# Optimization experiments

Hardware: AMD Instinct MI355X
Metric: run time of the kernel (lower is better)

Reference implementation:

```python
import jax, jax.numpy as jnp
import numpy as np

N, E, MB, H, FA, FB, HEADS, A_SIZE = 60000, 120000, 6, 128, 133, 147, 8, 20


def setup_inputs() -> dict:
    key = jax.random.key(0)
    ks = jax.random.split(key, 32)
    nrm = lambda k, s, sc: (jax.random.normal(k, s, jnp.float32) * sc)
    HD = HEADS * H
    inp = {
        "f_atoms": jax.random.normal(ks[0], (N, FA), jnp.float32),
        "f_bonds": jax.random.normal(ks[1], (E, FB), jnp.float32),
        "wi_atom": nrm(ks[2], (H, FA), 1 / np.sqrt(FA)),
        "wi_bond": nrm(ks[3], (H, FB), 1 / np.sqrt(FB)),
        "wh0": nrm(ks[4], (H, H), 1 / np.sqrt(H)),
        "wh1": nrm(ks[5], (H, H), 1 / np.sqrt(H)),
        "wh2": nrm(ks[6], (H, H), 1 / np.sqrt(H)),
        "q_w": nrm(ks[7], (HD, H), 1 / np.sqrt(H)),
        "q_b": nrm(ks[8], (HD,), 0.02),
        "k_w": nrm(ks[9], (HD, H), 1 / np.sqrt(H)),
        "k_b": nrm(ks[10], (HD,), 0.02),
        "v_w": nrm(ks[11], (HD, H), 1 / np.sqrt(H)),
        "v_b": nrm(ks[12], (HD,), 0.02),
        "e_w": nrm(ks[13], (HD, H), 1 / np.sqrt(H)),
        "skip_w": nrm(ks[14], (H, H), 1 / np.sqrt(H)),
        "skip_b": nrm(ks[15], (H,), 0.02),
        "lstm_wih": nrm(ks[16], (4 * H, 2 * H), 1 / np.sqrt(H)),
        "lstm_whh": nrm(ks[17], (4 * H, H), 1 / np.sqrt(H)),
        "lstm_bih": nrm(ks[18], (4 * H,), 1 / np.sqrt(H)),
        "lstm_bhh": nrm(ks[19], (4 * H,), 1 / np.sqrt(H)),
        "wo_w": nrm(ks[20], (H, 2 * H), 1 / np.sqrt(2 * H)),
        "wo_b": nrm(ks[21], (H,), 0.02),
        "a2b": jax.random.randint(ks[22], (N, MB), 0, E),
        "b2a": jax.random.randint(ks[23], (E,), 0, N),
        "b2revb": jax.random.randint(ks[24], (E,), 0, E),
        "bonds": jax.random.randint(ks[25], (2, E), 0, N),
        "a_size": A_SIZE,
    }
    return inp


def reference(f_atoms, f_bonds, wi_atom, wi_bond, wh0, wh1, wh2, q_w, q_b, k_w, k_b,
              v_w, v_b, e_w, skip_w, skip_b, lstm_wih, lstm_whh, lstm_bih, lstm_bhh,
              wo_w, wo_b, a2b, b2a, b2revb, bonds, a_size):
    relu = jax.nn.relu
    n = f_atoms.shape[0]
    h = wi_atom.shape[0]
    heads = q_w.shape[0] // h
    # input projections (bias=False) + activation
    input_atom = relu(f_atoms @ wi_atom.T)
    message_atom = input_atom
    input_bond = relu(f_bonds @ wi_bond.T)
    message_bond = input_bond
    # depth-1 = 3 message passing iterations (dropout p=0 -> identity)
    for wh in (wh0, wh1, wh2):
        nei = message_bond[a2b]                    # [N, max_nb, H] gather
        agg = nei.sum(axis=1) * nei.max(axis=1)    # fused sum*max aggregation
        message_atom = message_atom + agg
        mb = message_atom[b2a] - message_bond[b2revb]
        message_bond = relu(input_bond + mb @ wh.T)
    # TransformerConv(H, H, heads=8, concat=False, edge_dim=H)
    src, dst = bonds[0], bonds[1]
    e_num = src.shape[0]
    q = (message_atom @ q_w.T + q_b).reshape(n, heads, h)
    k = (message_atom @ k_w.T + k_b).reshape(n, heads, h)
    v = (message_atom @ v_w.T + v_b).reshape(n, heads, h)
    eattr = (message_bond @ e_w.T).reshape(e_num, heads, h)
    k_j = k[src] + eattr
    v_j = v[src] + eattr
    logits = (q[dst] * k_j).sum(-1) / jnp.sqrt(jnp.float32(h))  # [E, heads]
    m = jax.ops.segment_max(logits, dst, num_segments=n)
    m = jnp.where(jnp.isfinite(m), m, 0.0)
    ex = jnp.exp(logits - m[dst])
    denom = jax.ops.segment_sum(ex, dst, num_segments=n) + 1e-16
    alpha = ex / denom[dst]
    out = jax.ops.segment_sum(v_j * alpha[..., None], dst, num_segments=n)
    atom_hiddens = out.mean(axis=1) + (message_atom @ skip_w.T + skip_b)
    # Set2Set(T=1, num_layers=1) per molecule, vectorized over equal-size mols
    m_mols = n // a_size
    x = atom_hiddens.reshape(m_mols, a_size, h)
    hh = jnp.zeros((m_mols, h), jnp.float32)
    cc = jnp.zeros((m_mols, h), jnp.float32)
    q_star = jnp.zeros((m_mols, 2 * h), jnp.float32)
    gates = q_star @ lstm_wih.T + lstm_bih + hh @ lstm_whh.T + lstm_bhh
    gi, gf, gg, go = jnp.split(gates, 4, axis=-1)  # torch LSTM gate order i,f,g,o
    cc = jax.nn.sigmoid(gf) * cc + jax.nn.sigmoid(gi) * jnp.tanh(gg)
    qv = jax.nn.sigmoid(go) * jnp.tanh(cc)          # [M, H]
    e_att = (x * qv[:, None, :]).sum(-1)            # [M, A]
    a = jnp.exp(e_att - e_att.max(axis=1, keepdims=True))
    a = a / (a.sum(axis=1, keepdims=True) + 1e-16)
    r = jnp.einsum('ma,mah->mh', a, x)
    q_star = jnp.concatenate([qv, r], axis=-1)      # [M, 2H]
    return q_star @ wo_w.T + wo_b                   # [M, H]
```

## Files before the change

### kernel.cpp

```cpp
#include <hip/hip_runtime.h>
#include <hip/hip_bf16.h>

__global__ void zero_u32(unsigned int* __restrict__ p, long long n)
{
    long long i = (long long)blockIdx.x * 256 + threadIdx.x;
    if (i < n) p[i] = 0u;
}

__global__ void sentinel_f32(float* __restrict__ p, long long n, float v)
{
    long long i = (long long)blockIdx.x * 256 + threadIdx.x;
    if (i < n) p[i] = v;
}

__device__ __forceinline__ float4 load_f4_guard(const float* base, int gm, int M, int K, int kb)
{
    float4 v = make_float4(0.f, 0.f, 0.f, 0.f);
    if (gm < M) {
        const float* p = base + (size_t)gm * K + kb;
        if (kb + 4 <= K) v = *(const float4*)p;
        else {
            if (kb     < K) v.x = p[0];
            if (kb + 1 < K) v.y = p[1];
            if (kb + 2 < K) v.z = p[2];
            if (kb + 3 < K) v.w = p[3];
        }
    }
    return v;
}

struct GSeg {
    const float* A; const float* W; const float* bias; float* C;
    int M; int K; int bend;
};
struct GParams { GSeg s[4]; };

template<bool RELU>
__global__ __launch_bounds__(256) void gemm_multi(GParams P, int nseg)
{
    __shared__ float As[16][68];
    __shared__ float Ws[16][132];
    const int b = blockIdx.x;
    int si = 0, bbeg = 0;
    while (si + 1 < nseg && b >= P.s[si].bend) { bbeg = P.s[si].bend; ++si; }
    const GSeg S = P.s[si];
    const int tid = threadIdx.x;
    const int tx = tid & 15, ty = tid >> 4;
    const int row0 = (b - bbeg) * 64;
    const int r  = tid >> 2;
    const int k4 = (tid & 3) * 4;

    float acc[4][8] = {};
    for (int k0 = 0; k0 < S.K; k0 += 16) {
        {
            float4 av = load_f4_guard(S.A, row0 + r, S.M, S.K, k0 + k4);
            As[k4 + 0][r] = av.x; As[k4 + 1][r] = av.y;
            As[k4 + 2][r] = av.z; As[k4 + 3][r] = av.w;
        }
#pragma unroll
        for (int c = 0; c < 2; ++c) {
            int rr = r + c * 64;
            float4 wv = load_f4_guard(S.W, rr, 128, S.K, k0 + k4);
            Ws[k4 + 0][rr] = wv.x; Ws[k4 + 1][rr] = wv.y;
            Ws[k4 + 2][rr] = wv.z; Ws[k4 + 3][rr] = wv.w;
        }
        __syncthreads();
#pragma unroll
        for (int kk = 0; kk < 16; ++kk) {
            float4 a0 = *(const float4*)&As[kk][ty * 4];
            float4 w0 = *(const float4*)&Ws[kk][tx * 4];
            float4 w1 = *(const float4*)&Ws[kk][64 + tx * 4];
            float a[4] = {a0.x, a0.y, a0.z, a0.w};
            float w[8] = {w0.x, w0.y, w0.z, w0.w, w1.x, w1.y, w1.z, w1.w};
#pragma unroll
            for (int i = 0; i < 4; ++i)
#pragma unroll
                for (int j = 0; j < 8; ++j)
                    acc[i][j] += a[i] * w[j];
        }
        __syncthreads();
    }
    float bs[8];
    if (S.bias) {
#pragma unroll
        for (int j = 0; j < 4; ++j) {
            bs[j]     = S.bias[tx * 4 + j];
            bs[j + 4] = S.bias[64 + tx * 4 + j];
        }
    } else {
#pragma unroll
        for (int j = 0; j < 8; ++j) bs[j] = 0.f;
    }
#pragma unroll
    for (int i = 0; i < 4; ++i) {
        int gm = row0 + ty * 4 + i;
        if (gm >= S.M) continue;
#pragma unroll
        for (int jh = 0; jh < 2; ++jh) {
            float4 v;
            v.x = acc[i][jh * 4 + 0] + bs[jh * 4 + 0];
            v.y = acc[i][jh * 4 + 1] + bs[jh * 4 + 1];
            v.z = acc[i][jh * 4 + 2] + bs[jh * 4 + 2];
            v.w = acc[i][jh * 4 + 3] + bs[jh * 4 + 3];
            if (RELU) {
                v.x = fmaxf(v.x, 0.f); v.y = fmaxf(v.y, 0.f);
                v.z = fmaxf(v.z, 0.f); v.w = fmaxf(v.w, 0.f);
            }
            *(float4*)&S.C[(size_t)gm * 128 + jh * 64 + tx * 4] = v;
        }
    }
}

__global__ __launch_bounds__(256) void gemm_mp(
    const float* __restrict__ ma, const float* __restrict__ bond,
    const int* __restrict__ b2a, const int* __restrict__ b2revb,
    const float* __restrict__ inb, const float* __restrict__ wh,
    float* __restrict__ C)
{
    __shared__ float As[16][68];
    __shared__ float Ws[16][132];
    __shared__ int ia[64], ir[64];
    const int tid = threadIdx.x;
    const int tx = tid & 15, ty = tid >> 4;
    const int row0 = blockIdx.x * 64;
    const int r  = tid >> 2;
    const int k4 = (tid & 3) * 4;
    if (tid < 64)       ia[tid]      = b2a[row0 + tid];
    else if (tid < 128) ir[tid - 64] = b2revb[row0 + tid - 64];
    __syncthreads();
    float acc[4][8] = {};
    for (int k0 = 0; k0 < 128; k0 += 16) {
        {
            float4 x = *(const float4*)(ma   + (size_t)ia[r] * 128 + k0 + k4);
            float4 y = *(const float4*)(bond + (size_t)ir[r] * 128 + k0 + k4);
            As[k4 + 0][r] = x.x - y.x; As[k4 + 1][r] = x.y - y.y;
            As[k4 + 2][r] = x.z - y.z; As[k4 + 3][r] = x.w - y.w;
        }
#pragma unroll
        for (int c = 0; c < 2; ++c) {
            int rr = r + c * 64;
            float4 wv = *(const float4*)(wh + (size_t)rr * 128 + k0 + k4);
            Ws[k4 + 0][rr] = wv.x; Ws[k4 + 1][rr] = wv.y;
            Ws[k4 + 2][rr] = wv.z; Ws[k4 + 3][rr] = wv.w;
        }
        __syncthreads();
#pragma unroll
        for (int kk = 0; kk < 16; ++kk) {
            float4 a0 = *(const float4*)&As[kk][ty * 4];
            float4 w0 = *(const float4*)&Ws[kk][tx * 4];
            float4 w1 = *(const float4*)&Ws[kk][64 + tx * 4];
            float a[4] = {a0.x, a0.y, a0.z, a0.w};
            float w[8] = {w0.x, w0.y, w0.z, w0.w, w1.x, w1.y, w1.z, w1.w};
#pragma unroll
            for (int i = 0; i < 4; ++i)
#pragma unroll
                for (int j = 0; j < 8; ++j)
                    acc[i][j] += a[i] * w[j];
        }
        __syncthreads();
    }
#pragma unroll
    for (int i = 0; i < 4; ++i) {
        int gm = row0 + ty * 4 + i;
#pragma unroll
        for (int jh = 0; jh < 2; ++jh) {
            int cc = jh * 64 + tx * 4;
            float4 o = *(const float4*)&inb[(size_t)gm * 128 + cc];
            float4 v;
            v.x = fmaxf(acc[i][jh * 4 + 0] + o.x, 0.f);
            v.y = fmaxf(acc[i][jh * 4 + 1] + o.y, 0.f);
            v.z = fmaxf(acc[i][jh * 4 + 2] + o.z, 0.f);
            v.w = fmaxf(acc[i][jh * 4 + 3] + o.w, 0.f);
            *(float4*)&C[(size_t)gm * 128 + cc] = v;
        }
    }
}

__global__ __launch_bounds__(256) void agg_kernel(
    const float* __restrict__ bond, const int* __restrict__ a2b,
    float* __restrict__ ma, int N)
{
    int n = blockIdx.x * 8 + (threadIdx.x >> 5);
    if (n >= N) return;
    int d4 = (threadIdx.x & 31) * 4;
    const int* ix = a2b + (size_t)n * 6;
    float4 s = make_float4(0.f, 0.f, 0.f, 0.f);
    float4 mx = make_float4(-3.0e38f, -3.0e38f, -3.0e38f, -3.0e38f);
#pragma unroll
    for (int j = 0; j < 6; ++j) {
        float4 v = *(const float4*)(bond + (size_t)ix[j] * 128 + d4);
        s.x += v.x; s.y += v.y; s.z += v.z; s.w += v.w;
        mx.x = fmaxf(mx.x, v.x); mx.y = fmaxf(mx.y, v.y);
        mx.z = fmaxf(mx.z, v.z); mx.w = fmaxf(mx.w, v.w);
    }
    float* mp = ma + (size_t)n * 128 + d4;
    float4 o = *(const float4*)mp;
    o.x += s.x * mx.x; o.y += s.y * mx.y; o.z += s.z * mx.z; o.w += s.w * mx.w;
    *(float4*)mp = o;
}

__global__ void count_kernel(const int* __restrict__ dst, int* __restrict__ counts, int E)
{
    int e = blockIdx.x * 256 + threadIdx.x;
    if (e < E) atomicAdd(&counts[dst[e]], 1);
}

__global__ __launch_bounds__(1024) void scan_kernel(
    const int* __restrict__ counts, int* __restrict__ offsets, int N)
{
    __shared__ int sums[1024];
    int t = threadIdx.x;
    int chunk = (N + 1023) >> 10;
    int b = t * chunk;
    int e = b + chunk; if (e > N) e = N;
    int s = 0;
    for (int i = b; i < e; ++i) s += counts[i];
    sums[t] = s;
    __syncthreads();
    for (int off = 1; off < 1024; off <<= 1) {
        int v = (t >= off) ? sums[t - off] : 0;
        __syncthreads();
        sums[t] += v;
        __syncthreads();
    }
    int run = sums[t] - s;
    for (int i = b; i < e; ++i) { offsets[i] = run; run += counts[i]; }
    if (t == 1023) offsets[N] = sums[1023];
}

__global__ void fill_kernel(const int* __restrict__ dst, const int* __restrict__ offsets,
                            int* __restrict__ cursor, int* __restrict__ elist, int E)
{
    int e = blockIdx.x * 256 + threadIdx.x;
    if (e < E) {
        int d = dst[e];
        int pos = offsets[d] + atomicAdd(&cursor[d], 1);
        elist[pos] = e;
    }
}

__global__ __launch_bounds__(256) void attn_pass1(
    const float* __restrict__ qh, const float* __restrict__ kh,
    const float* __restrict__ eh, const int* __restrict__ srcA,
    const int* __restrict__ offs, const int* __restrict__ elist,
    float* __restrict__ alpha, int N)
{
    int n = blockIdx.x * 4 + (threadIdx.x >> 6);
    if (n >= N) return;
    int l = threadIdx.x & 63;
    const float rs = 0.08838834764831845f;
    float2 q2 = ((const float2*)(qh + (size_t)n * 128))[l];
    int b = offs[n], en = offs[n + 1];
    float m = -3.0e38f, denom = 0.f;
    int ie = b;
    for (; ie + 2 <= en; ie += 2) {
        int e0 = elist[ie], e1 = elist[ie + 1];
        int s0 = srcA[e0], s1 = srcA[e1];
        float2 k0v = ((const float2*)(kh + (size_t)s0 * 128))[l];
        float2 e0v = ((const float2*)(eh + (size_t)e0 * 128))[l];
        float2 k1v = ((const float2*)(kh + (size_t)s1 * 128))[l];
        float2 e1v = ((const float2*)(eh + (size_t)e1 * 128))[l];
        float p0 = q2.x * (k0v.x + e0v.x) + q2.y * (k0v.y + e0v.y);
        float p1 = q2.x * (k1v.x + e1v.x) + q2.y * (k1v.y + e1v.y);
        p0 += __shfl_xor(p0, 1);  p1 += __shfl_xor(p1, 1);
        p0 += __shfl_xor(p0, 2);  p1 += __shfl_xor(p1, 2);
        p0 += __shfl_xor(p0, 4);  p1 += __shfl_xor(p1, 4);
        p0 += __shfl_xor(p0, 8);  p1 += __shfl_xor(p1, 8);
        p0 += __shfl_xor(p0, 16); p1 += __shfl_xor(p1, 16);
        p0 += __shfl_xor(p0, 32); p1 += __shfl_xor(p1, 32);
        float l0 = p0 * rs, l1 = p1 * rs;
        if (l == 0) { alpha[ie] = l0; alpha[ie + 1] = l1; }
        float mn = fmaxf(m, fmaxf(l0, l1));
        float sc = __expf(m - mn);
        denom = denom * sc + __expf(l0 - mn) + __expf(l1 - mn);
        m = mn;
    }
    if (ie < en) {
        int e0 = elist[ie];
        int s0 = srcA[e0];
        float2 k0v = ((const float2*)(kh + (size_t)s0 * 128))[l];
        float2 e0v = ((const float2*)(eh + (size_t)e0 * 128))[l];
        float p0 = q2.x * (k0v.x + e0v.x) + q2.y * (k0v.y + e0v.y);
        p0 += __shfl_xor(p0, 1);  p0 += __shfl_xor(p0, 2);
        p0 += __shfl_xor(p0, 4);  p0 += __shfl_xor(p0, 8);
        p0 += __shfl_xor(p0, 16); p0 += __shfl_xor(p0, 32);
        float l0 = p0 * rs;
        if (l == 0) alpha[ie] = l0;
        float mn = fmaxf(m, l0);
        denom = denom * __expf(m - mn) + __expf(l0 - mn);
        m = mn;
    }
    if (l == 0 && b < en) {
        float invd = 1.f / (denom + 1e-16f);
        for (int i = b; i < en; ++i)
            alpha[i] = __expf(alpha[i] - m) * invd;
    }
}

__global__ __launch_bounds__(256) void attn_pass2(
    const float* __restrict__ vh, const float* __restrict__ eh,
    const int* __restrict__ srcA, const int* __restrict__ offs,
    const int* __restrict__ elist, const float* __restrict__ alpha,
    float* __restrict__ outsum, int N)
{
    int n = blockIdx.x * 4 + (threadIdx.x >> 6);
    if (n >= N) return;
    int l = threadIdx.x & 63;
    int b = offs[n], en = offs[n + 1];
    float a0 = 0.f, a1 = 0.f;
    int ie = b;
    for (; ie + 2 <= en; ie += 2) {
        int e0 = elist[ie], e1 = elist[ie + 1];
        int s0 = srcA[e0], s1 = srcA[e1];
        float al0 = alpha[ie], al1 = alpha[ie + 1];
        float2 v0 = ((const float2*)(vh + (size_t)s0 * 128))[l];
        float2 e0v = ((const float2*)(eh + (size_t)e0 * 128))[l];
        float2 v1 = ((const float2*)(vh + (size_t)s1 * 128))[l];
        float2 e1v = ((const float2*)(eh + (size_t)e1 * 128))[l];
        a0 += al0 * (v0.x + e0v.x) + al1 * (v1.x + e1v.x);
        a1 += al0 * (v0.y + e0v.y) + al1 * (v1.y + e1v.y);
    }
    if (ie < en) {
        int e0 = elist[ie];
        int s0 = srcA[e0];
        float al0 = alpha[ie];
        float2 v0 = ((const float2*)(vh + (size_t)s0 * 128))[l];
        float2 e0v = ((const float2*)(eh + (size_t)e0 * 128))[l];
        a0 += al0 * (v0.x + e0v.x);
        a1 += al0 * (v0.y + e0v.y);
    }
    float* op = outsum + (size_t)n * 128 + 2 * l;
    op[0] += 0.125f * a0;
    op[1] += 0.125f * a1;
}

__global__ void qv_kernel(const float* __restrict__ bih, const float* __restrict__ bhh,
                          float* __restrict__ qv)
{
    int t = threadIdx.x;
    float gi = bih[t] + bhh[t];
    float gg = bih[256 + t] + bhh[256 + t];
    float go = bih[384 + t] + bhh[384 + t];
    float sig_i = 1.f / (1.f + __expf(-gi));
    float c = sig_i * tanhf(gg);
    float sig_o = 1.f / (1.f + __expf(-go));
    qv[t] = sig_o * tanhf(c);
}

__global__ __launch_bounds__(256) void s2s_kernel(
    const float* __restrict__ ah, const float* __restrict__ qv,
    const float* __restrict__ wo_w, const float* __restrict__ wo_b,
    float* __restrict__ out, int M)
{
    __shared__ float rsh[4][128];
    __shared__ float qsh[128];
    int wv = threadIdx.x >> 6, l = threadIdx.x & 63;
    if (threadIdx.x < 128) qsh[threadIdx.x] = qv[threadIdx.x];
    __syncthreads();
    int m = blockIdx.x * 4 + wv;
    bool active = (m < M);
    if (active) {
        const float* x = ah + (size_t)m * 20 * 128;
        float q0 = qsh[2 * l], q1 = qsh[2 * l + 1];
        float e[20]; float mx = -3.0e38f;
#pragma unroll
        for (int a = 0; a < 20; ++a) {
            float part = x[a * 128 + 2 * l] * q0 + x[a * 128 + 2 * l + 1] * q1;
            part += __shfl_xor(part, 1);  part += __shfl_xor(part, 2);
            part += __shfl_xor(part, 4);  part += __shfl_xor(part, 8);
            part += __shfl_xor(part, 16); part += __shfl_xor(part, 32);
            e[a] = part; mx = fmaxf(mx, part);
        }
        float sum = 0.f;
#pragma unroll
        for (int a = 0; a < 20; ++a) { e[a] = __expf(e[a] - mx); sum += e[a]; }
        float invs = 1.f / (sum + 1e-16f);
        float r0 = 0.f, r1 = 0.f;
#pragma unroll
        for (int a = 0; a < 20; ++a) {
            float w = e[a] * invs;
            r0 += w * x[a * 128 + 2 * l];
            r1 += w * x[a * 128 + 2 * l + 1];
        }
        rsh[wv][2 * l] = r0; rsh[wv][2 * l + 1] = r1;
    }
    __syncthreads();
    if (active) {
#pragma unroll
        for (int dd = 0; dd < 2; ++dd) {
            int d = 2 * l + dd;
            float acc = wo_b[d];
            const float* wr = wo_w + (size_t)d * 256;
            for (int j = 0; j < 128; ++j)
                acc += wr[j] * qsh[j] + wr[128 + j] * rsh[wv][j];
            out[(size_t)m * 128 + d] = acc;
        }
    }
}

extern "C" void kernel_launch(void* const* d_in, const int* in_sizes, int n_in,
                              void* d_out, int out_size, void* d_ws, size_t ws_size,
                              hipStream_t stream)
{
    const int N = 60000, E = 120000, FA = 133, FB = 147;
    const float* f_atoms  = (const float*)d_in[0];
    const float* f_bonds  = (const float*)d_in[1];
    const float* wi_atom  = (const float*)d_in[2];
    const float* wi_bond  = (const float*)d_in[3];
    const float* wh[3]    = { (const float*)d_in[4], (const float*)d_in[5], (const float*)d_in[6] };
    const float* q_w      = (const float*)d_in[7];
    const float* q_b      = (const float*)d_in[8];
    const float* k_w      = (const float*)d_in[9];
    const float* k_b      = (const float*)d_in[10];
    const float* v_w      = (const float*)d_in[11];
    const float* v_b      = (const float*)d_in[12];
    const float* e_w      = (const float*)d_in[13];
    const float* skip_w   = (const float*)d_in[14];
    const float* skip_b   = (const float*)d_in[15];
    const float* lstm_bih = (const float*)d_in[18];
    const float* lstm_bhh = (const float*)d_in[19];
    const float* wo_w     = (const float*)d_in[20];
    const float* wo_b     = (const float*)d_in[21];
    const int* a2b    = (const int*)d_in[22];
    const int* b2a    = (const int*)d_in[23];
    const int* b2revb = (const int*)d_in[24];
    const int* bonds  = (const int*)d_in[25];
    const int* srcA = bonds;
    const int* dstA = bonds + E;

    const size_t NB = (size_t)N * 128;
    const size_t EB = (size_t)E * 128;
    char* ws = (char*)d_ws;
    size_t off = 0;
    auto alloc = [&](size_t bytes) -> char* {
        char* p = ws + off; off += (bytes + 255) & ~255ULL; return p;
    };
    float* msg_atom = (float*)alloc(NB * 4);
    float* B1       = (float*)alloc(EB * 4);
    float* B2       = (float*)alloc(EB * 4);
    float* B3       = (float*)alloc(EB * 4);
    float* outsum   = (float*)alloc(NB * 4);
    float* alpha    = (float*)alloc((size_t)E * 4);
    int* counts  = (int*)alloc((size_t)N * 2 * 4);
    int* cursor  = counts + N;
    int* offsets = (int*)alloc((size_t)(N + 1) * 4);
    int* elist   = (int*)alloc((size_t)E * 4);
    float* qvb   = (float*)alloc(128 * 4);

    if (off > ws_size) {
        long long n = out_size;
        sentinel_f32<<<(int)((n + 255) / 256), 256, 0, stream>>>((float*)d_out, n, 1.0e9f);
        return;
    }

    float* q_h = B1;
    float* k_h = B1 + NB;
    float* v_h = B1;
    float* e_h = B3;

    const int gN64 = (N + 63) / 64;
    const int gE64 = E / 64;

    zero_u32<<<(2 * N + 255) / 256, 256, 0, stream>>>((unsigned int*)counts, 2 * N);

    {
        GParams P{};
        P.s[0] = { f_atoms, wi_atom, nullptr, msg_atom, N, FA, gN64 };
        P.s[1] = { f_bonds, wi_bond, nullptr, B1,       E, FB, gN64 + gE64 };
        gemm_multi<true><<<gN64 + gE64, 256, 0, stream>>>(P, 2);
    }

    count_kernel<<<(E + 255) / 256, 256, 0, stream>>>(dstA, counts, E);
    scan_kernel<<<1, 1024, 0, stream>>>(counts, offsets, N);
    fill_kernel<<<(E + 255) / 256, 256, 0, stream>>>(dstA, offsets, cursor, elist, E);

    const float* cur = B1;
    float* nxt[3] = { B2, B3, B2 };
    for (int it = 0; it < 3; ++it) {
        agg_kernel<<<(N + 7) / 8, 256, 0, stream>>>(cur, a2b, msg_atom, N);
        gemm_mp<<<gE64, 256, 0, stream>>>(
            msg_atom, cur, b2a, b2revb, B1, wh[it], nxt[it]);
        cur = nxt[it];
    }

    for (int h = 0; h < 8; ++h) {
        const size_t w_off = (size_t)h * 128 * 128;
        GParams P{};
        P.s[0] = { B2,       e_w + w_off, nullptr,        e_h, E, 128, gE64 };
        P.s[1] = { msg_atom, q_w + w_off, q_b + h * 128,  q_h, N, 128, gE64 + gN64 };
        P.s[2] = { msg_atom, k_w + w_off, k_b + h * 128,  k_h, N, 128, gE64 + 2 * gN64 };
        int nseg = 3, nblk = gE64 + 2 * gN64;
        if (h == 0) {
            P.s[3] = { msg_atom, skip_w, skip_b, outsum, N, 128, gE64 + 3 * gN64 };
            nseg = 4; nblk += gN64;
        }
        gemm_multi<false><<<nblk, 256, 0, stream>>>(P, nseg);
        attn_pass1<<<(N + 3) / 4, 256, 0, stream>>>(
            q_h, k_h, e_h, srcA, offsets, elist, alpha, N);
        {
            GParams PV{};
            PV.s[0] = { msg_atom, v_w + w_off, v_b + h * 128, v_h, N, 128, gN64 };
            gemm_multi<false><<<gN64, 256, 0, stream>>>(PV, 1);
        }
        attn_pass2<<<(N + 3) / 4, 256, 0, stream>>>(
            v_h, e_h, srcA, offsets, elist, alpha, outsum, N);
    }

    qv_kernel<<<1, 128, 0, stream>>>(lstm_bih, lstm_bhh, qvb);
    const int M = N / 20;
    s2s_kernel<<<(M + 3) / 4, 256, 0, stream>>>(outsum, qvb, wo_w, wo_b, (float*)d_out, M);
}
```

Measured before the change: 2.235 ms.

## Fuse attention passes and apply V projection after aggregation

Merges the two attention passes into one kernel and removes the per-head V GEMM. Using linearity, the alpha-weighted sum of source atom messages is aggregated first, then multiplied by a transposed V weight held per head, with the bias scaled by the alpha sum. This drops a GEMM over all atoms per head and one kernel launch per head. In exchange, every wave now runs a 128x128 matvec that reads weights from global memory, and the block needs a __syncthreads.

```diff
diff --git a/kernel.cpp b/kernel.cpp
--- a/kernel.cpp
+++ b/kernel.cpp
@@ -11,6 +11,15 @@
 {
     long long i = (long long)blockIdx.x * 256 + threadIdx.x;
     if (i < n) p[i] = v;
+}
+
+__global__ __launch_bounds__(128) void wt_kernel(const float* __restrict__ vw,
+                                                 float* __restrict__ WT)
+{
+    int hd = blockIdx.x;
+    int h = hd >> 7, d = hd & 127;
+    int i = threadIdx.x;
+    WT[((size_t)h * 128 + i) * 128 + d] = vw[(size_t)hd * 128 + i];
 }
 
 __device__ __forceinline__ float4 load_f4_guard(const float* base, int gm, int M, int K, int kb)
@@ -239,99 +248,71 @@
     }
 }
 
-__global__ __launch_bounds__(256) void attn_pass1(
+__global__ __launch_bounds__(256) void attn_fused(
     const float* __restrict__ qh, const float* __restrict__ kh,
-    const float* __restrict__ eh, const int* __restrict__ srcA,
-    const int* __restrict__ offs, const int* __restrict__ elist,
-    float* __restrict__ alpha, int N)
-{
-    int n = blockIdx.x * 4 + (threadIdx.x >> 6);
-    if (n >= N) return;
+    const float* __restrict__ eh, const float* __restrict__ ma,
+    const float* __restrict__ vb, const float* __restrict__ WTh,
+    const int* __restrict__ srcA, const int* __restrict__ offs,
+    const int* __restrict__ elist, float* __restrict__ logitbuf,
+    float* __restrict__ outsum, int N)
+{
+    __shared__ float zsh[4][130];
+    int wv = threadIdx.x >> 6;
+    int n = blockIdx.x * 4 + wv;
     int l = threadIdx.x & 63;
     const float rs = 0.08838834764831845f;
-    float2 q2 = ((const float2*)(qh + (size_t)n * 128))[l];
-    int b = offs[n], en = offs[n + 1];
     float m = -3.0e38f, denom = 0.f;
-    int ie = b;
-    for (; ie + 2 <= en; ie += 2) {
-        int e0 = elist[ie], e1 = elist[ie + 1];
-        int s0 = srcA[e0], s1 = srcA[e1];
-        float2 k0v = ((const float2*)(kh + (size_t)s0 * 128))[l];
-        float2 e0v = ((const float2*)(eh + (size_t)e0 * 128))[l];
-        float2 k1v = ((const float2*)(kh + (size_t)s1 * 128))[l];
-        float2 e1v = ((const float2*)(eh + (size_t)e1 * 128))[l];
-        float p0 = q2.x * (k0v.x + e0v.x) + q2.y * (k0v.y + e0v.y);
-        float p1 = q2.x * (k1v.x + e1v.x) + q2.y * (k1v.y + e1v.y);
-        p0 += __shfl_xor(p0, 1);  p1 += __shfl_xor(p1, 1);
-        p0 += __shfl_xor(p0, 2);  p1 += __shfl_xor(p1, 2);
-        p0 += __shfl_xor(p0, 4);  p1 += __shfl_xor(p1, 4);
-        p0 += __shfl_xor(p0, 8);  p1 += __shfl_xor(p1, 8);
-        p0 += __shfl_xor(p0, 16); p1 += __shfl_xor(p1, 16);
-        p0 += __shfl_xor(p0, 32); p1 += __shfl_xor(p1, 32);
-        float l0 = p0 * rs, l1 = p1 * rs;
-        if (l == 0) { alpha[ie] = l0; alpha[ie + 1] = l1; }
-        float mn = fmaxf(m, fmaxf(l0, l1));
-        float sc = __expf(m - mn);
-        denom = denom * sc + __expf(l0 - mn) + __expf(l1 - mn);
+    int b = 0, en = 0;
+    float2 q2 = make_float2(0.f, 0.f);
+    if (n < N) {
+        q2 = ((const float2*)(qh + (size_t)n * 128))[l];
+        b = offs[n]; en = offs[n + 1];
+    }
+    for (int ie = b; ie < en; ++ie) {
+        int e = elist[ie];
+        int s = srcA[e];
+        float2 k2 = ((const float2*)(kh + (size_t)s * 128))[l];
+        float2 e2 = ((const float2*)(eh + (size_t)e * 128))[l];
+        float p = q2.x * (k2.x + e2.x) + q2.y * (k2.y + e2.y);
+        p += __shfl_xor(p, 1);  p += __shfl_xor(p, 2);
+        p += __shfl_xor(p, 4);  p += __shfl_xor(p, 8);
+        p += __shfl_xor(p, 16); p += __shfl_xor(p, 32);
+        float lg = p * rs;
+        if (l == 0) logitbuf[ie] = lg;
+        float mn = fmaxf(m, lg);
+        denom = denom * __expf(m - mn) + __expf(lg - mn);
         m = mn;
     }
-    if (ie < en) {
-        int e0 = elist[ie];
-        int s0 = srcA[e0];
-        float2 k0v = ((const float2*)(kh + (size_t)s0 * 128))[l];
-        float2 e0v = ((const float2*)(eh + (size_t)e0 * 128))[l];
-        float p0 = q2.x * (k0v.x + e0v.x) + q2.y * (k0v.y + e0v.y);
-        p0 += __shfl_xor(p0, 1);  p0 += __shfl_xor(p0, 2);
-        p0 += __shfl_xor(p0, 4);  p0 += __shfl_xor(p0, 8);
-        p0 += __shfl_xor(p0, 16); p0 += __shfl_xor(p0, 32);
-        float l0 = p0 * rs;
-        if (l == 0) alpha[ie] = l0;
-        float mn = fmaxf(m, l0);
-        denom = denom * __expf(m - mn) + __expf(l0 - mn);
-        m = mn;
-    }
-    if (l == 0 && b < en) {
-        float invd = 1.f / (denom + 1e-16f);
-        for (int i = b; i < en; ++i)
-            alpha[i] = __expf(alpha[i] - m) * invd;
-    }
-}
-
-__global__ __launch_bounds__(256) void attn_pass2(
-    const float* __restrict__ vh, const float* __restrict__ eh,
-    const int* __restrict__ srcA, const int* __restrict__ offs,
-    const int* __restrict__ elist, const float* __restrict__ alpha,
-    float* __restrict__ outsum, int N)
-{
-    int n = blockIdx.x * 4 + (threadIdx.x >> 6);
-    if (n >= N) return;
-    int l = threadIdx.x & 63;
-    int b = offs[n], en = offs[n + 1];
-    float a0 = 0.f, a1 = 0.f;
-    int ie = b;
-    for (; ie + 2 <= en; ie += 2) {
-        int e0 = elist[ie], e1 = elist[ie + 1];
-        int s0 = srcA[e0], s1 = srcA[e1];
-        float al0 = alpha[ie], al1 = alpha[ie + 1];
-        float2 v0 = ((const float2*)(vh + (size_t)s0 * 128))[l];
-        float2 e0v = ((const float2*)(eh + (size_t)e0 * 128))[l];
-        float2 v1 = ((const float2*)(vh + (size_t)s1 * 128))[l];
-        float2 e1v = ((const float2*)(eh + (size_t)e1 * 128))[l];
-        a0 += al0 * (v0.x + e0v.x) + al1 * (v1.x + e1v.x);
-        a1 += al0 * (v0.y + e0v.y) + al1 * (v1.y + e1v.y);
-    }
-    if (ie < en) {
-        int e0 = elist[ie];
-        int s0 = srcA[e0];
-        float al0 = alpha[ie];
-        float2 v0 = ((const float2*)(vh + (size_t)s0 * 128))[l];
-        float2 e0v = ((const float2*)(eh + (size_t)e0 * 128))[l];
-        a0 += al0 * (v0.x + e0v.x);
-        a1 += al0 * (v0.y + e0v.y);
-    }
-    float* op = outsum + (size_t)n * 128 + 2 * l;
-    op[0] += 0.125f * a0;
-    op[1] += 0.125f * a1;
+    float invd = 1.f / (denom + 1e-16f);
+    float sa = denom * invd;
+    float z0 = 0.f, z1 = 0.f, a0 = 0.f, a1 = 0.f;
+    for (int ie = b; ie < en; ++ie) {
+        int e = elist[ie];
+        int s = srcA[e];
+        float lg = (l == 0) ? logitbuf[ie] : 0.f;
+        lg = __shfl(lg, 0);
+        float al = __expf(lg - m) * invd;
+        float2 m2 = ((const float2*)(ma + (size_t)s * 128))[l];
+        float2 e2 = ((const float2*)(eh + (size_t)e * 128))[l];
+        z0 += al * m2.x; z1 += al * m2.y;
+        a0 += al * e2.x; a1 += al * e2.y;
+    }
+    zsh[wv][2 * l]     = z0;
+    zsh[wv][2 * l + 1] = z1;
+    __syncthreads();
+    float o0 = 0.f, o1 = 0.f;
+#pragma unroll 4
+    for (int i = 0; i < 128; ++i) {
+        float zi = zsh[wv][i];
+        float2 w2 = ((const float2*)(WTh + (size_t)i * 128))[l];
+        o0 += zi * w2.x; o1 += zi * w2.y;
+    }
+    if (n < N) {
+        float vb0 = vb[2 * l], vb1 = vb[2 * l + 1];
+        float* op = outsum + (size_t)n * 128 + 2 * l;
+        op[0] += 0.125f * (a0 + sa * vb0 + o0);
+        op[1] += 0.125f * (a1 + sa * vb1 + o1);
+    }
 }
 
 __global__ void qv_kernel(const float* __restrict__ bih, const float* __restrict__ bhh,
@@ -446,6 +427,7 @@
     int* offsets = (int*)alloc((size_t)(N + 1) * 4);
     int* elist   = (int*)alloc((size_t)E * 4);
     float* qvb   = (float*)alloc(128 * 4);
+    float* WT    = (float*)alloc((size_t)8 * 128 * 128 * 4);
 
     if (off > ws_size) {
         long long n = out_size;
@@ -455,13 +437,13 @@
 
     float* q_h = B1;
     float* k_h = B1 + NB;
-    float* v_h = B1;
     float* e_h = B3;
 
     const int gN64 = (N + 63) / 64;
     const int gE64 = E / 64;
 
     zero_u32<<<(2 * N + 255) / 256, 256, 0, stream>>>((unsigned int*)counts, 2 * N);
+    wt_kernel<<<1024, 128, 0, stream>>>(v_w, WT);
 
     {
         GParams P{};
@@ -495,15 +477,9 @@
             nseg = 4; nblk += gN64;
         }
         gemm_multi<false><<<nblk, 256, 0, stream>>>(P, nseg);
-        attn_pass1<<<(N + 3) / 4, 256, 0, stream>>>(
-            q_h, k_h, e_h, srcA, offsets, elist, alpha, N);
-        {
-            GParams PV{};
-            PV.s[0] = { msg_atom, v_w + w_off, v_b + h * 128, v_h, N, 128, gN64 };
-            gemm_multi<false><<<gN64, 256, 0, stream>>>(PV, 1);
-        }
-        attn_pass2<<<(N + 3) / 4, 256, 0, stream>>>(
-            v_h, e_h, srcA, offsets, elist, alpha, outsum, N);
+        attn_fused<<<(N + 3) / 4, 256, 0, stream>>>(
+            q_h, k_h, e_h, msg_atom, v_b + h * 128, WT + (size_t)h * 16384,
+            srcA, offsets, elist, alpha, outsum, N);
     }
 
     qv_kernel<<<1, 128, 0, stream>>>(lstm_bih, lstm_bhh, qvb);
```

After: 3.499 ms. +56.5%, slower.
